# Kernel optimization log

Measured on AMD Instinct MI355X. Metric: run time of the kernel, lower is better.

The kernel has to match this reference:

```python
import jax, jax.numpy as jnp
import numpy as np
import math

# ---- cfg constants (PUMA functional model defaults) ----
XBAR_ROW, XBAR_COL = 128, 128
GON, GOFF, VMAX = 1.0 / 100.0, 1.0 / 600.0, 0.25  # cancel exactly in ideal ADC decode
BIT_SLICE, BIT_STREAM = 2, 1
WEIGHT_BITS, INPUT_BITS = 16, 16
W_FRAC = WEIGHT_BITS // 4 * 3   # 12 fractional bits (default -1 path)
I_FRAC = INPUT_BITS // 4 * 3    # 12
ACM_BITS = 16
ACM_FRAC = ACM_BITS // 4 * 3    # 12 -> accumulator range [-8, 8)
ADC_BIT = int(math.log2(XBAR_ROW)) + BIT_SLICE  # 7 + 2 = 9 (bit_stream==1 adds nothing)
NSLICE = 2 ** BIT_SLICE - 1     # conductance states per slice
NS = WEIGHT_BITS // BIT_SLICE   # 8 weight slices, MSB first
NB = INPUT_BITS // BIT_STREAM   # 16 input bit streams, LSB first


def bit_slicing(w):
    # w: [out, in] nonnegative -> [in, out*NS]; per output col, NS slices MSB first
    wint = jnp.clip(jnp.round(w * 2.0 ** W_FRAC), 0.0, 2.0 ** WEIGHT_BITS - 1)
    shifts = 2.0 ** (BIT_SLICE * jnp.arange(NS - 1, -1, -1, dtype=jnp.float32))
    sl = jnp.floor(wint[:, :, None] / shifts) % (2 ** BIT_SLICE)  # [out,in,NS]
    return sl.transpose(1, 0, 2).reshape(w.shape[1], w.shape[0] * NS)


def to_bits(x):
    # two's-complement fixed-point bits, LSB first -> [B, in, NB]
    xint = jnp.clip(jnp.round(x * 2.0 ** I_FRAC), -(2.0 ** (INPUT_BITS - 1)), 2.0 ** (INPUT_BITS - 1) - 1)
    xint = jnp.where(xint < 0, xint + 2.0 ** INPUT_BITS, xint)
    shifts = 2.0 ** jnp.arange(INPUT_BITS, dtype=jnp.float32)
    return jnp.floor(xint[:, :, None] / shifts) % 2.0


def tile(ws, rt, ct):
    # pad [rows, cols] to crossbar tiles [rt, ct, XBAR_ROW, XBAR_COL]
    pad = jnp.zeros((rt * XBAR_ROW, ct * XBAR_COL), ws.dtype)
    pad = pad.at[:ws.shape[0], :ws.shape[1]].set(ws)
    return pad.reshape(rt, XBAR_ROW, ct, XBAR_COL).transpose(0, 2, 1, 3)


def quant_acm(v):
    lim = 2.0 ** (ACM_BITS - ACM_FRAC - 1)
    q = jnp.round(v * 2.0 ** ACM_FRAC) / 2.0 ** ACM_FRAC
    return jnp.clip(q, -lim, lim - 2.0 ** (-ACM_FRAC))


def crossbar_mvm(bits, slices):
    # bits: [B, R, 128, NB] in {0,1}; slices: [R, C, 128, 128] in {0..NSLICE}
    G = slices * (GON - GOFF) / NSLICE + GOFF          # conductance mapping
    V = bits * VMAX                                     # DAC (1-bit streams)
    # analog column currents per stream: [B, R, C, NB, 128]
    I = jnp.einsum('brks,rckj->brcsj', V, G)
    vsum = V.sum(2)                                     # [B, R, NB]
    # ideal decode: remove Goff offset, rescale to integer dot counts
    counts = (I - vsum[:, :, None, :, None] * GOFF) / (VMAX * (GON - GOFF) / NSLICE)
    # ADC quantization over full-scale range xbar_row*NSLICE with 2**ADC_BIT levels
    step = (XBAR_ROW * NSLICE) / (2.0 ** ADC_BIT - 1)
    counts = jnp.round(counts / step) * step
    B, R, C = counts.shape[:3]
    counts = counts.reshape(B, R, C, NB, XBAR_COL // NS, NS)
    slice_w = 2.0 ** (BIT_SLICE * jnp.arange(NS - 1, -1, -1, dtype=jnp.float32))
    psum = (counts * slice_w).sum(-1)                   # shift-add slices -> [B,R,C,NB,cols]
    stream_w = 2.0 ** jnp.arange(NB, dtype=jnp.float32)
    stream_w = stream_w.at[-1].multiply(-1.0)           # two's-complement MSB is negative
    out = (psum * stream_w[:, None]).sum(3)             # shift-add streams -> [B,R,C,cols]
    out = quant_acm(out / 2.0 ** (W_FRAC + I_FRAC))     # back to float, accumulator quant
    out = out.sum(1)                                    # digital sum over row tiles
    return out.reshape(B, C * (XBAR_COL // NS))


def mvm_forward(x, weight):
    out_f, in_f = weight.shape
    pos = bit_slicing(jnp.clip(weight, 0.0, None))
    neg = bit_slicing(jnp.abs(jnp.clip(weight, None, 0.0)))
    rt = -(-pos.shape[0] // XBAR_ROW)
    ct = -(-pos.shape[1] // XBAR_COL)
    xb_pos, xb_neg = tile(pos, rt, ct), tile(neg, rt, ct)
    bits = to_bits(x)                                   # [B, in, NB]
    B = x.shape[0]
    bits_p = jnp.zeros((B, rt * XBAR_ROW, NB), x.dtype).at[:, :in_f].set(bits)
    bits_p = bits_p.reshape(B, rt, XBAR_ROW, NB)
    out = crossbar_mvm(bits_p, xb_pos) - crossbar_mvm(bits_p, xb_neg)
    return out[:, :out_f]


def setup_inputs() -> dict:
    key = jax.random.key(0)
    k1, k2, k3 = jax.random.split(key, 3)
    x = jax.random.normal(k1, (512, 1024), dtype=jnp.float32) * 0.1
    weight = jax.random.normal(k2, (128, 1024), dtype=jnp.float32) * 0.05
    bias = jax.random.uniform(k3, (128,), dtype=jnp.float32, minval=-0.1, maxval=0.1)
    return {"x": x, "weight": weight, "bias": bias}


def reference(x, weight, bias):
    return mvm_forward(x, weight) + bias[None, :]
```

## Files before the change

kernel.cpp:

```cpp
#include <hip/hip_runtime.h>
#include <stdint.h>

typedef __attribute__((ext_vector_type(4)))  int i32x4;
typedef __attribute__((ext_vector_type(16))) int i32x16;

#define XM_OFF 0u
#define BP_OFF 1048576u
#define PT_OFF 3145728u

__device__ __forceinline__ uint32_t q16(float v){
  float f = fminf(fmaxf(rintf(v*4096.f), -32768.f), 32767.f);
  return (uint32_t)(int)f & 0xffffu;
}

__global__ __launch_bounds__(256) void pack_k(const float* __restrict__ x, const float* __restrict__ w,
                                              uint4* __restrict__ xm, uint32_t* __restrict__ Bw){
  const int lane = threadIdx.x & 63;
  if (blockIdx.x < 1024){
    int wv = blockIdx.x*4 + (threadIdx.x >> 6);
    int b = wv >> 3, z = wv & 7;
    const float* xp = x + b*1024 + z*128;
    uint32_t u0 = q16(xp[lane]);
    uint32_t u1 = q16(xp[lane + 64]);
    uint4 out4 = {0,0,0,0};
    #pragma unroll
    for (int s = 0; s < 16; ++s){
      unsigned long long m0 = __ballot((u0 >> s) & 1u);
      unsigned long long m1 = __ballot((u1 >> s) & 1u);
      if (lane == s){
        out4.x = (uint32_t)m0; out4.y = (uint32_t)(m0 >> 32);
        out4.z = (uint32_t)m1; out4.w = (uint32_t)(m1 >> 32);
      }
    }
    if (lane < 16) xm[(b*8 + z)*16 + lane] = out4;
  } else {
    int t = (blockIdx.x - 1024)*256 + threadIdx.x;
    int j = t >> 8, kq = t & 255;
    int r = kq >> 5, kd = kq & 31;
    float4 v = *reinterpret_cast<const float4*>(w + j*1024 + kq*4);
    #pragma unroll
    for (int p = 0; p < 2; ++p){
      uint32_t q0 = (uint32_t)fminf(rintf(fmaxf(p ? -v.x : v.x, 0.f)*4096.f), 65535.f);
      uint32_t q1 = (uint32_t)fminf(rintf(fmaxf(p ? -v.y : v.y, 0.f)*4096.f), 65535.f);
      uint32_t q2 = (uint32_t)fminf(rintf(fmaxf(p ? -v.z : v.z, 0.f)*4096.f), 65535.f);
      uint32_t q3 = (uint32_t)fminf(rintf(fmaxf(p ? -v.w : v.w, 0.f)*4096.f), 65535.f);
      #pragma unroll
      for (int sl = 0; sl < 8; ++sl){
        int sh = 2*(7 - sl);
        uint32_t word = ((q0 >> sh) & 3u) | (((q1 >> sh) & 3u) << 8)
                      | (((q2 >> sh) & 3u) << 16) | (((q3 >> sh) & 3u) << 24);
        Bw[(((r*2 + p)*8 + sl)*128 + j)*32 + kd] = word;
      }
    }
  }
}

__global__ __launch_bounds__(512, 4) void mvm_main_k(const uint4* __restrict__ xm,
                                                     const uint8_t* __restrict__ Bp,
                                                     float* __restrict__ partial){
  __shared__ uint8_t lds[65536];
  __shared__ uint32_t flg[8];
  const int tid = threadIdx.x, lane = tid & 63, wid = tid >> 6;
  const int z = blockIdx.z, jblk = blockIdx.y;
  const int col = lane & 31, hi = lane >> 5;

  {
    const int q = lane >> 3, cS = (lane & 7) ^ q;
    uint32_t f2 = 0;
    #pragma unroll
    for (int u = 0; u < 2; ++u){
      const int si = wid + u*8;
      const uint8_t* src = Bp + ((size_t)((z*16 + si)*128 + jblk*32) << 7);
      uint4 r0 = *(const uint4*)(src + (q     )*128 + cS*16);
      uint4 r1 = *(const uint4*)(src + (q +  8)*128 + cS*16);
      uint4 r2 = *(const uint4*)(src + (q + 16)*128 + cS*16);
      uint4 r3 = *(const uint4*)(src + (q + 24)*128 + cS*16);
      uint8_t* dst = lds + si*4096 + lane*16;
      *(uint4*)(dst       ) = r0;
      *(uint4*)(dst + 1024) = r1;
      *(uint4*)(dst + 2048) = r2;
      *(uint4*)(dst + 3072) = r3;
      uint32_t o = r0.x|r0.y|r0.z|r0.w | r1.x|r1.y|r1.z|r1.w
                 | r2.x|r2.y|r2.z|r2.w | r3.x|r3.y|r3.z|r3.w;
      f2 |= (__any(o != 0u) ? 1u : 0u) << u;
    }
    if (lane == 0) flg[wid] = f2;
  }

  const int bb  = blockIdx.x*32 + wid*4;
  const int s_a = lane & 15;
  const uint4 pwA = xm[((bb     + (col >> 4))*8 + z)*16 + s_a];
  const uint4 pwB = xm[((bb + 2 + (col >> 4))*8 + z)*16 + s_a];
  i32x4 afrA[4], afrB[4];
  {
    const uint32_t wA[4] = {pwA.x, pwA.y, pwA.z, pwA.w};
    const uint32_t wB[4] = {pwB.x, pwB.y, pwB.z, pwB.w};
    #pragma unroll
    for (int f = 0; f < 4; ++f){
      uint32_t plA = wA[f] >> (hi*16);
      uint32_t plB = wB[f] >> (hi*16);
      #pragma unroll
      for (int wI = 0; wI < 4; ++wI){
        afrA[f][wI] = (int)((((plA >> (wI*4)) & 0xFu) * 0x204081u) & 0x01010101u);
        afrB[f][wI] = (int)((((plB >> (wI*4)) & 0xFu) * 0x204081u) & 0x01010101u);
      }
    }
  }
  __syncthreads();

  uint32_t msk = 0;
  #pragma unroll
  for (int w2 = 0; w2 < 8; ++w2){
    uint32_t f2 = flg[w2];
    msk |= (f2 & 1u) << w2;
    msk |= ((f2 >> 1) & 1u) << (w2 + 8);
  }
  msk = (uint32_t)__builtin_amdgcn_readfirstlane((int)msk);

  const int c7 = col & 7;
  const int xo0 = ((0 + hi) ^ c7) << 4;
  const int xo1 = ((2 + hi) ^ c7) << 4;
  const int xo2 = ((4 + hi) ^ c7) << 4;
  const int xo3 = ((6 + hi) ^ c7) << 4;

  i32x16 zz;
  #pragma unroll
  for (int i = 0; i < 16; ++i) zz[i] = 0;

  const float C1 = (float)(511.0/384.0);
  const float QC = (float)(384.0/511.0/4096.0);
  const float sc = hi ? 16.0f : 1.0f;
  const float w7 = hi ? -8.0f : 8.0f;
  float oA0 = 0.f, oA1 = 0.f, oB0 = 0.f, oB1 = 0.f;

#define EPI(cc, A0, A1) do { \
    float nf[16]; \
    _Pragma("unroll") \
    for (int g_ = 0; g_ < 16; ++g_) nf[g_] = rintf((float)cc[g_] * C1); \
    float t0 = fmaf(nf[1], 2.f, nf[0]);  t0 = fmaf(nf[2], 4.f, t0);  t0 = fmaf(nf[3], 8.f, t0); \
    float t1 = fmaf(nf[5], 2.f, nf[4]);  t1 = fmaf(nf[6], 4.f, t1);  t1 = fmaf(nf[7], w7, t1); \
    float t2 = fmaf(nf[9], 2.f, nf[8]);  t2 = fmaf(nf[10],4.f, t2);  t2 = fmaf(nf[11],8.f, t2); \
    float t3 = fmaf(nf[13],2.f, nf[12]); t3 = fmaf(nf[14],4.f, t3);  t3 = fmaf(nf[15],w7, t3); \
    A0 = fmaf(t0, slwv, A0);  A0 = fmaf(t1, slw256, A0); \
    A1 = fmaf(t2, slwv, A1);  A1 = fmaf(t3, slw256, A1); \
  } while (0)

  #pragma unroll
  for (int p = 0; p < 2; ++p){
    float aA0 = 0.f, aA1 = 0.f, aB0 = 0.f, aB1 = 0.f;
    #pragma unroll
    for (int sl = 0; sl < 8; ++sl){
      const int ti = p*8 + sl;
      if (msk & (1u << ti)){
        const float slwv   = (float)(1 << (14 - 2*sl));
        const float slw256 = slwv * 256.0f;
        const uint8_t* lb = lds + ti*4096 + col*128;
        i32x4 b0 = *(const i32x4*)(lb + xo0);
        i32x4 b1 = *(const i32x4*)(lb + xo1);
        i32x4 b2 = *(const i32x4*)(lb + xo2);
        i32x4 b3 = *(const i32x4*)(lb + xo3);
        i32x16 cc = __builtin_amdgcn_mfma_i32_32x32x32_i8(afrA[0], b0, zz, 0, 0, 0);
        cc = __builtin_amdgcn_mfma_i32_32x32x32_i8(afrA[1], b1, cc, 0, 0, 0);
        cc = __builtin_amdgcn_mfma_i32_32x32x32_i8(afrA[2], b2, cc, 0, 0, 0);
        cc = __builtin_amdgcn_mfma_i32_32x32x32_i8(afrA[3], b3, cc, 0, 0, 0);
        i32x16 cd = __builtin_amdgcn_mfma_i32_32x32x32_i8(afrB[0], b0, zz, 0, 0, 0);
        cd = __builtin_amdgcn_mfma_i32_32x32x32_i8(afrB[1], b1, cd, 0, 0, 0);
        cd = __builtin_amdgcn_mfma_i32_32x32x32_i8(afrB[2], b2, cd, 0, 0, 0);
        cd = __builtin_amdgcn_mfma_i32_32x32x32_i8(afrB[3], b3, cd, 0, 0, 0);
        EPI(cc, aA0, aA1);
        EPI(cd, aB0, aB1);
      }
    }

    aA0 *= sc; aA1 *= sc; aB0 *= sc; aB1 *= sc;
    aA0 += __shfl_xor(aA0, 32); aA1 += __shfl_xor(aA1, 32);
    aB0 += __shfl_xor(aB0, 32); aB1 += __shfl_xor(aB1, 32);

    float qA0 = fminf(fmaxf(rintf(aA0*QC)*(1.0f/4096.0f), -8.0f), 8.0f - 1.0f/4096.0f);
    float qA1 = fminf(fmaxf(rintf(aA1*QC)*(1.0f/4096.0f), -8.0f), 8.0f - 1.0f/4096.0f);
    float qB0 = fminf(fmaxf(rintf(aB0*QC)*(1.0f/4096.0f), -8.0f), 8.0f - 1.0f/4096.0f);
    float qB1 = fminf(fmaxf(rintf(aB1*QC)*(1.0f/4096.0f), -8.0f), 8.0f - 1.0f/4096.0f);
    if (p == 0){ oA0 += qA0; oA1 += qA1; oB0 += qB0; oB1 += qB1; }
    else       { oA0 -= qA0; oA1 -= qA1; oB0 -= qB0; oB1 -= qB1; }
  }
#undef EPI

  const int jout = jblk*32 + col;
  partial[(z*512 + bb + hi    )*128 + jout] = hi ? oA1 : oA0;
  partial[(z*512 + bb + 2 + hi)*128 + jout] = hi ? oB1 : oB0;
}

__global__ __launch_bounds__(256) void reduce_k(const float* __restrict__ partial,
                                                const float* __restrict__ bias,
                                                float* __restrict__ out){
  int t = blockIdx.x*256 + threadIdx.x;
  int b = t >> 7, j = t & 127;
  float s = 0.f;
  #pragma unroll
  for (int z = 0; z < 8; ++z) s += partial[(z*512 + b)*128 + j];
  out[t] = s + bias[j];
}

extern "C" void kernel_launch(void* const* d_in, const int* in_sizes, int n_in,
                              void* d_out, int out_size, void* d_ws, size_t ws_size,
                              hipStream_t stream){
  const float* x    = (const float*)d_in[0];
  const float* w    = (const float*)d_in[1];
  const float* bias = (const float*)d_in[2];
  uint8_t* ws = (uint8_t*)d_ws;

  hipLaunchKernelGGL(pack_k, dim3(1152), dim3(256), 0, stream,
                     x, w, (uint4*)(ws + XM_OFF), (uint32_t*)(ws + BP_OFF));
  hipLaunchKernelGGL(mvm_main_k, dim3(16, 4, 8), dim3(512), 0, stream,
                     (const uint4*)(ws + XM_OFF), ws + BP_OFF, (float*)(ws + PT_OFF));
  hipLaunchKernelGGL(reduce_k, dim3(256), dim3(256), 0, stream,
                     (const float*)(ws + PT_OFF), bias, (float*)d_out);
}
```

Measured before the change: 26.93 us.

## Precompute nonzero slice masks in pack kernel and skip loading empty tiles

The weight-pack kernel now records which (row tile, column block) slice tiles are nonzero through a shuffle reduction and an atomicOr into a small mask buffer, which is cleared by a memset. The main kernel reads this mask up front, skips global-to-LDS loads for all-zero slice tiles, and no longer needs the LDS flag exchange. The MFMA chains are also split per output pair with s_setprio raised around them, to interleave matrix work with the epilogue across waves. The cost is an extra memset launch plus atomics in the pack kernel.

```diff
diff --git a/kernel.cpp b/kernel.cpp
--- a/kernel.cpp
+++ b/kernel.cpp
@@ -6,7 +6,8 @@
 
 #define XM_OFF 0u
 #define BP_OFF 1048576u
-#define PT_OFF 3145728u
+#define MK_OFF 3145728u
+#define PT_OFF 3149824u
 
 __device__ __forceinline__ uint32_t q16(float v){
   float f = fminf(fmaxf(rintf(v*4096.f), -32768.f), 32767.f);
@@ -14,7 +15,8 @@
 }
 
 __global__ __launch_bounds__(256) void pack_k(const float* __restrict__ x, const float* __restrict__ w,
-                                              uint4* __restrict__ xm, uint32_t* __restrict__ Bw){
+                                              uint4* __restrict__ xm, uint32_t* __restrict__ Bw,
+                                              uint32_t* __restrict__ mask){
   const int lane = threadIdx.x & 63;
   if (blockIdx.x < 1024){
     int wv = blockIdx.x*4 + (threadIdx.x >> 6);
@@ -38,6 +40,7 @@
     int j = t >> 8, kq = t & 255;
     int r = kq >> 5, kd = kq & 31;
     float4 v = *reinterpret_cast<const float4*>(w + j*1024 + kq*4);
+    uint32_t lm = 0;
     #pragma unroll
     for (int p = 0; p < 2; ++p){
       uint32_t q0 = (uint32_t)fminf(rintf(fmaxf(p ? -v.x : v.x, 0.f)*4096.f), 65535.f);
@@ -50,41 +53,47 @@
         uint32_t word = ((q0 >> sh) & 3u) | (((q1 >> sh) & 3u) << 8)
                       | (((q2 >> sh) & 3u) << 16) | (((q3 >> sh) & 3u) << 24);
         Bw[(((r*2 + p)*8 + sl)*128 + j)*32 + kd] = word;
-      }
-    }
+        lm |= (word != 0u ? 1u : 0u) << (p*8 + sl);
+      }
+    }
+    lm |= (uint32_t)__shfl_xor((int)lm, 16);
+    lm |= (uint32_t)__shfl_xor((int)lm, 8);
+    lm |= (uint32_t)__shfl_xor((int)lm, 4);
+    lm |= (uint32_t)__shfl_xor((int)lm, 2);
+    lm |= (uint32_t)__shfl_xor((int)lm, 1);
+    if ((threadIdx.x & 31) == 0) atomicOr(&mask[r*4 + (j >> 5)], lm);
   }
 }
 
 __global__ __launch_bounds__(512, 4) void mvm_main_k(const uint4* __restrict__ xm,
                                                      const uint8_t* __restrict__ Bp,
+                                                     const uint32_t* __restrict__ mask,
                                                      float* __restrict__ partial){
   __shared__ uint8_t lds[65536];
-  __shared__ uint32_t flg[8];
   const int tid = threadIdx.x, lane = tid & 63, wid = tid >> 6;
   const int z = blockIdx.z, jblk = blockIdx.y;
   const int col = lane & 31, hi = lane >> 5;
 
+  const uint32_t msk = (uint32_t)__builtin_amdgcn_readfirstlane((int)(mask[z*4 + jblk] & 0xFFFFu));
+
   {
     const int q = lane >> 3, cS = (lane & 7) ^ q;
-    uint32_t f2 = 0;
     #pragma unroll
     for (int u = 0; u < 2; ++u){
       const int si = wid + u*8;
-      const uint8_t* src = Bp + ((size_t)((z*16 + si)*128 + jblk*32) << 7);
-      uint4 r0 = *(const uint4*)(src + (q     )*128 + cS*16);
-      uint4 r1 = *(const uint4*)(src + (q +  8)*128 + cS*16);
-      uint4 r2 = *(const uint4*)(src + (q + 16)*128 + cS*16);
-      uint4 r3 = *(const uint4*)(src + (q + 24)*128 + cS*16);
-      uint8_t* dst = lds + si*4096 + lane*16;
-      *(uint4*)(dst       ) = r0;
-      *(uint4*)(dst + 1024) = r1;
-      *(uint4*)(dst + 2048) = r2;
-      *(uint4*)(dst + 3072) = r3;
-      uint32_t o = r0.x|r0.y|r0.z|r0.w | r1.x|r1.y|r1.z|r1.w
-                 | r2.x|r2.y|r2.z|r2.w | r3.x|r3.y|r3.z|r3.w;
-      f2 |= (__any(o != 0u) ? 1u : 0u) << u;
-    }
-    if (lane == 0) flg[wid] = f2;
+      if (msk & (1u << si)){
+        const uint8_t* src = Bp + ((size_t)((z*16 + si)*128 + jblk*32) << 7);
+        uint4 r0 = *(const uint4*)(src + (q     )*128 + cS*16);
+        uint4 r1 = *(const uint4*)(src + (q +  8)*128 + cS*16);
+        uint4 r2 = *(const uint4*)(src + (q + 16)*128 + cS*16);
+        uint4 r3 = *(const uint4*)(src + (q + 24)*128 + cS*16);
+        uint8_t* dst = lds + si*4096 + lane*16;
+        *(uint4*)(dst       ) = r0;
+        *(uint4*)(dst + 1024) = r1;
+        *(uint4*)(dst + 2048) = r2;
+        *(uint4*)(dst + 3072) = r3;
+      }
+    }
   }
 
   const int bb  = blockIdx.x*32 + wid*4;
@@ -107,15 +116,6 @@
     }
   }
   __syncthreads();
-
-  uint32_t msk = 0;
-  #pragma unroll
-  for (int w2 = 0; w2 < 8; ++w2){
-    uint32_t f2 = flg[w2];
-    msk |= (f2 & 1u) << w2;
-    msk |= ((f2 >> 1) & 1u) << (w2 + 8);
-  }
-  msk = (uint32_t)__builtin_amdgcn_readfirstlane((int)msk);
 
   const int c7 = col & 7;
   const int xo0 = ((0 + hi) ^ c7) << 4;
@@ -159,16 +159,24 @@
         i32x4 b1 = *(const i32x4*)(lb + xo1);
         i32x4 b2 = *(const i32x4*)(lb + xo2);
         i32x4 b3 = *(const i32x4*)(lb + xo3);
-        i32x16 cc = __builtin_amdgcn_mfma_i32_32x32x32_i8(afrA[0], b0, zz, 0, 0, 0);
-        cc = __builtin_amdgcn_mfma_i32_32x32x32_i8(afrA[1], b1, cc, 0, 0, 0);
-        cc = __builtin_amdgcn_mfma_i32_32x32x32_i8(afrA[2], b2, cc, 0, 0, 0);
-        cc = __builtin_amdgcn_mfma_i32_32x32x32_i8(afrA[3], b3, cc, 0, 0, 0);
-        i32x16 cd = __builtin_amdgcn_mfma_i32_32x32x32_i8(afrB[0], b0, zz, 0, 0, 0);
-        cd = __builtin_amdgcn_mfma_i32_32x32x32_i8(afrB[1], b1, cd, 0, 0, 0);
-        cd = __builtin_amdgcn_mfma_i32_32x32x32_i8(afrB[2], b2, cd, 0, 0, 0);
-        cd = __builtin_amdgcn_mfma_i32_32x32x32_i8(afrB[3], b3, cd, 0, 0, 0);
-        EPI(cc, aA0, aA1);
-        EPI(cd, aB0, aB1);
+        {
+          __builtin_amdgcn_s_setprio(1);
+          i32x16 cc = __builtin_amdgcn_mfma_i32_32x32x32_i8(afrA[0], b0, zz, 0, 0, 0);
+          cc = __builtin_amdgcn_mfma_i32_32x32x32_i8(afrA[1], b1, cc, 0, 0, 0);
+          cc = __builtin_amdgcn_mfma_i32_32x32x32_i8(afrA[2], b2, cc, 0, 0, 0);
+          cc = __builtin_amdgcn_mfma_i32_32x32x32_i8(afrA[3], b3, cc, 0, 0, 0);
+          __builtin_amdgcn_s_setprio(0);
+          EPI(cc, aA0, aA1);
+        }
+        {
+          __builtin_amdgcn_s_setprio(1);
+          i32x16 cd = __builtin_amdgcn_mfma_i32_32x32x32_i8(afrB[0], b0, zz, 0, 0, 0);
+          cd = __builtin_amdgcn_mfma_i32_32x32x32_i8(afrB[1], b1, cd, 0, 0, 0);
+          cd = __builtin_amdgcn_mfma_i32_32x32x32_i8(afrB[2], b2, cd, 0, 0, 0);
+          cd = __builtin_amdgcn_mfma_i32_32x32x32_i8(afrB[3], b3, cd, 0, 0, 0);
+          __builtin_amdgcn_s_setprio(0);
+          EPI(cd, aB0, aB1);
+        }
       }
     }
 
@@ -209,10 +217,12 @@
   const float* bias = (const float*)d_in[2];
   uint8_t* ws = (uint8_t*)d_ws;
 
+  hipMemsetAsync(ws + MK_OFF, 0, 128, stream);
   hipLaunchKernelGGL(pack_k, dim3(1152), dim3(256), 0, stream,
-                     x, w, (uint4*)(ws + XM_OFF), (uint32_t*)(ws + BP_OFF));
+                     x, w, (uint4*)(ws + XM_OFF), (uint32_t*)(ws + BP_OFF), (uint32_t*)(ws + MK_OFF));
   hipLaunchKernelGGL(mvm_main_k, dim3(16, 4, 8), dim3(512), 0, stream,
-                     (const uint4*)(ws + XM_OFF), ws + BP_OFF, (float*)(ws + PT_OFF));
+                     (const uint4*)(ws + XM_OFF), ws + BP_OFF,
+                     (const uint32_t*)(ws + MK_OFF), (float*)(ws + PT_OFF));
   hipLaunchKernelGGL(reduce_k, dim3(256), dim3(256), 0, stream,
                      (const float*)(ws + PT_OFF), bias, (float*)d_out);
 }
```

Result: slower. 33.28 us (+23.6%).
